# Kernel tuning notes

Measured on AMD Instinct MI355X. Metric: run time of the kernel, lower is better.

The kernel has to match this reference:

```python
import jax, jax.numpy as jnp
import numpy as np
from jax import lax

G = 16          # deform_groups
K = 9           # 3x3 kernel points
MAX_RES = 10.0  # max_residue_magnitude
PAD = 1         # stride=1, padding=1, dilation=1


def _leaky(x):
    return jnp.where(x >= 0, x, 0.1 * x)


def _conv3x3(x, w, b):
    y = lax.conv_general_dilated(x, w, (1, 1), ((PAD, PAD), (PAD, PAD)),
                                 dimension_numbers=('NCHW', 'OIHW', 'NCHW'))
    return y + b[None, :, None, None]


def _deform_conv2d(x, offset, mask, weight, bias):
    # x: [B,Cin,H,W]; offset: [B,2*G*K,H,W]; mask: [B,G*K,H,W]
    B, Cin, H, W = x.shape
    cpg = Cin // G
    Cout = weight.shape[0]
    # torchvision layout: [B, G, K, 2(y,x), H, W]
    off = offset.reshape(B, G, K, 2, H, W)
    ky = (jnp.arange(K) // 3 - PAD).astype(x.dtype).reshape(1, 1, K, 1, 1)
    kx = (jnp.arange(K) % 3 - PAD).astype(x.dtype).reshape(1, 1, K, 1, 1)
    py = jnp.arange(H, dtype=x.dtype).reshape(1, 1, 1, H, 1) + ky + off[:, :, :, 0]  # [B,G,K,H,W]
    px = jnp.arange(W, dtype=x.dtype).reshape(1, 1, 1, 1, W) + kx + off[:, :, :, 1]
    y0f = jnp.floor(py)
    x0f = jnp.floor(px)
    wy = py - y0f
    wx = px - x0f
    y0 = y0f.astype(jnp.int32)
    x0 = x0f.astype(jnp.int32)

    xf = x.reshape(B, G, cpg, H * W)
    # gather per (batch, group): xg [cpg, H*W], idx [K,H,W] -> [cpg,K,H,W]
    gather_fn = jax.vmap(jax.vmap(lambda xg, idx: jnp.take(xg, idx, axis=1)))

    def corner(yi, xi):
        valid = (yi >= 0) & (yi < H) & (xi >= 0) & (xi < W)   # zero padding outside
        idx = jnp.clip(yi, 0, H - 1) * W + jnp.clip(xi, 0, W - 1)
        v = gather_fn(xf, idx)                                # [B,G,cpg,K,H,W]
        return v * valid[:, :, None].astype(x.dtype)

    val = (corner(y0, x0) * ((1 - wy) * (1 - wx))[:, :, None]
           + corner(y0, x0 + 1) * ((1 - wy) * wx)[:, :, None]
           + corner(y0 + 1, x0) * (wy * (1 - wx))[:, :, None]
           + corner(y0 + 1, x0 + 1) * (wy * wx)[:, :, None])
    val = val * mask.reshape(B, G, 1, K, H, W)                # modulation
    wr = weight.reshape(Cout, G, cpg, K)
    return jnp.einsum('ogck,bgckhw->bohw', wr, val) + bias[None, :, None, None]


def _forward(x, extra_feat, flow_1, flow_2, w1, b1, w2, b2, w3, b3, w4, b4, dcn_w, dcn_b):
    ef = jnp.concatenate([extra_feat, flow_1, flow_2], axis=1)
    h = _leaky(_conv3x3(ef, w1, b1))
    h = _leaky(_conv3x3(h, w2, b2))
    h = _leaky(_conv3x3(h, w3, b3))
    out = _conv3x3(h, w4, b4)                 # [B, 27*G, H, W]
    o1, o2, m = jnp.split(out, 3, axis=1)
    offset = MAX_RES * jnp.tanh(jnp.concatenate([o1, o2], axis=1))
    off1, off2 = jnp.split(offset, 2, axis=1)
    rep = off1.shape[1] // 2
    off1 = off1 + jnp.tile(flow_1[:, ::-1], (1, rep, 1, 1))   # flip(1): (x,y)->(y,x)
    off2 = off2 + jnp.tile(flow_2[:, ::-1], (1, rep, 1, 1))
    offset = jnp.concatenate([off1, off2], axis=1)
    mask = jax.nn.sigmoid(m)
    return _deform_conv2d(x, offset, mask, dcn_w, dcn_b)


def setup_inputs() -> dict:
    key = jax.random.key(0)
    ks = jax.random.split(key, 10)
    B, H, W = 2, 128, 128
    Cin, Cout = 128, 64
    n = lambda k, s, sc=1.0: jax.random.normal(k, s, dtype=jnp.float32) * sc
    return {
        'x': n(ks[0], (B, Cin, H, W)),
        'extra_feat': n(ks[1], (B, 3 * Cout, H, W)),
        'flow_1': n(ks[2], (B, 2, H, W)),
        'flow_2': n(ks[3], (B, 2, H, W)),
        'w1': n(ks[4], (Cout, 3 * Cout + 4, 3, 3), 0.02), 'b1': jnp.zeros((Cout,), jnp.float32),
        'w2': n(ks[5], (Cout, Cout, 3, 3), 0.05), 'b2': jnp.zeros((Cout,), jnp.float32),
        'w3': n(ks[6], (Cout, Cout, 3, 3), 0.05), 'b3': jnp.zeros((Cout,), jnp.float32),
        'w4': n(ks[7], (27 * G, Cout, 3, 3), 0.01), 'b4': jnp.zeros((27 * G,), jnp.float32),
        'dcn_w': n(ks[8], (Cout, Cin, 3, 3), 0.05), 'dcn_b': jnp.zeros((Cout,), jnp.float32),
    }


def reference(x, extra_feat, flow_1, flow_2, w1, b1, w2, b2, w3, b3, w4, b4, dcn_w, dcn_b):
    return _forward(x, extra_feat, flow_1, flow_2, w1, b1, w2, b2, w3, b3, w4, b4, dcn_w, dcn_b)
```

## Files before the change

### kernel.cpp

```cpp
#include <hip/hip_runtime.h>
#include <math.h>

namespace {
constexpr int H = 128, W = 128, NB = 2;
constexpr int HW = H * W;
constexpr int WP = 130, HP = 130, HWP = WP * HP;
constexpr int NTHR = 256;
constexpr int DG = 16, CPG = 8, DCN_CIN = 128, DCN_COUT = 64;

constexpr size_t OFF_HA  = 0;
constexpr size_t OFF_HB  = 2163200;
constexpr size_t OFF_PIN = 4326400;
constexpr size_t OFF_O4  = 4194304;
constexpr size_t OFF_XT  = 0;
}

__global__ __launch_bounds__(NTHR) void prep_k(
    const float* __restrict__ ef, const float* __restrict__ f1,
    const float* __restrict__ f2,
    float* __restrict__ pin, float* __restrict__ hA, float* __restrict__ hB)
{
  constexpr int PACK_N  = NB * 196 * HW;
  constexpr int BORD_CH = NB * (196 + 64 + 64);
  constexpr int BORD_N  = BORD_CH * 516;
  const int total = PACK_N + BORD_N;
  for (int gid = blockIdx.x * NTHR + threadIdx.x; gid < total;
       gid += gridDim.x * NTHR) {
    if (gid < PACK_N) {
      const int b = gid / (196 * HW);
      const int r = gid - b * 196 * HW;
      const int c = r / HW;
      const int p = r - c * HW;
      const int y = p / W, x = p - y * W;
      float v;
      if (c < 192)      v = ef[(b * 192 + c) * HW + p];
      else if (c < 194) v = f1[(b * 2 + (c - 192)) * HW + p];
      else              v = f2[(b * 2 + (c - 194)) * HW + p];
      pin[(size_t)(b * 196 + c) * HWP + (y + 1) * WP + (x + 1)] = v;
    } else {
      const int k  = gid - PACK_N;
      const int ch = k / 516;
      const int e  = k - ch * 516;
      float* base;
      if (ch < NB * 196)            base = pin + (size_t)ch * HWP;
      else if (ch < NB * 196 + NB * 64) base = hA + (size_t)(ch - NB * 196) * HWP;
      else                          base = hB + (size_t)(ch - NB * 196 - NB * 64) * HWP;
      int off;
      if (e < 260) { const int rr = (e < 130) ? 0 : (HP - 1); off = rr * WP + (e % 130); }
      else { const int e2 = e - 260; const int y = 1 + (e2 & 127); off = y * WP + ((e2 < 128) ? 0 : (WP - 1)); }
      base[off] = 0.f;
    }
  }
}

template<int CIN, int COUT, int CC, int EPI>
__global__ __launch_bounds__(NTHR) void conv3x3_k(
    const float* __restrict__ in,
    const float* __restrict__ wt,
    const float* __restrict__ bias,
    const float* __restrict__ fl1, const float* __restrict__ fl2,
    float* __restrict__ out)
{
  constexpr int NST = 2;
  constexpr int HHW = 34, HN = HHW * HHW;
  constexpr int IN_E = NST * HN;
  constexpr int J_IN = (IN_E + NTHR - 1) / NTHR;
  constexpr int WT_E = CC * NST * 9;
  constexpr int J_WT = (WT_E + NTHR - 1) / NTHR;
  constexpr int R = CIN / NST;

  __shared__ float s_in[2][NST * HN];
  __shared__ float s_wt[2][CC * NST * 12];

  const int t    = threadIdx.x;
  const int tile = blockIdx.x;
  const int tx0  = (tile & 3) * 32, ty0 = (tile >> 2) * 32;
  const int oc0  = blockIdx.y * CC;
  const int b    = blockIdx.z;
  const int px0  = (t & 15) * 2;
  const int py0  = (t >> 4) * 2;

  const float* inB = in + (size_t)b * CIN * HWP;

  int iadr[J_IN]; bool ivl[J_IN];
  #pragma unroll
  for (int j = 0; j < J_IN; ++j) {
    const int idx = j * NTHR + t;
    ivl[j] = idx < IN_E;
    const int ii = idx / HN, rem = idx - ii * HN;
    const int hy = rem / HHW, hx = rem - hy * HHW;
    iadr[j] = ivl[j] ? (ii * HWP + (ty0 + hy) * WP + (tx0 + hx)) : 0;
  }
  int wadr[J_WT], wl[J_WT]; bool wvl[J_WT];
  #pragma unroll
  for (int j = 0; j < J_WT; ++j) {
    const int idx = j * NTHR + t;
    wvl[j] = idx < WT_E;
    const int o = idx / (NST * 9), r2 = idx - o * (NST * 9), ii = r2 / 9, k = r2 - ii * 9;
    wadr[j] = wvl[j] ? (((oc0 + o) * CIN + ii) * 9 + k) : 0;
    wl[j]   = wvl[j] ? ((o * NST + ii) * 12 + k) : 0;
  }

  float rin[J_IN], rwt[J_WT], acc[CC][4];
  #pragma unroll
  for (int o = 0; o < CC; ++o)
    #pragma unroll
    for (int p = 0; p < 4; ++p) acc[o][p] = 0.f;

  #pragma unroll
  for (int j = 0; j < J_IN; ++j) if (ivl[j]) rin[j] = inB[iadr[j]];
  #pragma unroll
  for (int j = 0; j < J_WT; ++j) if (wvl[j]) rwt[j] = wt[wadr[j]];

  for (int r = 0; r < R; ++r) {
    float* si = s_in[r & 1];
    float* sw = s_wt[r & 1];
    #pragma unroll
    for (int j = 0; j < J_IN; ++j) if (ivl[j]) si[j * NTHR + t] = rin[j];
    #pragma unroll
    for (int j = 0; j < J_WT; ++j) if (wvl[j]) sw[wl[j]] = rwt[j];
    __syncthreads();
    if (r + 1 < R) {
      const float* ip = inB + (size_t)(r + 1) * NST * HWP;
      const float* wp = wt + (size_t)(r + 1) * NST * 9;
      #pragma unroll
      for (int j = 0; j < J_IN; ++j) if (ivl[j]) rin[j] = ip[iadr[j]];
      #pragma unroll
      for (int j = 0; j < J_WT; ++j) if (wvl[j]) rwt[j] = wp[wadr[j]];
    }
    #pragma unroll
    for (int i = 0; i < NST; ++i) {
      float va[16];
      #pragma unroll
      for (int dy = 0; dy < 4; ++dy)
        #pragma unroll
        for (int dx = 0; dx < 4; ++dx)
          va[dy * 4 + dx] = si[i * HN + (py0 + dy) * HHW + (px0 + dx)];
      #pragma unroll
      for (int o = 0; o < CC; ++o) {
        const float* wr = &sw[(o * NST + i) * 12];
        float w[9];
        #pragma unroll
        for (int k = 0; k < 9; ++k) w[k] = wr[k];
        #pragma unroll
        for (int py = 0; py < 2; ++py)
          #pragma unroll
          for (int px = 0; px < 2; ++px) {
            float a = acc[o][py * 2 + px];
            #pragma unroll
            for (int ky = 0; ky < 3; ++ky)
              #pragma unroll
              for (int kx = 0; kx < 3; ++kx)
                a = fmaf(va[(py + ky) * 4 + (px + kx)], w[ky * 3 + kx], a);
            acc[o][py * 2 + px] = a;
          }
      }
    }
  }

  if (EPI == 2) {
    float flo[2][2][2][2];
    #pragma unroll
    for (int py = 0; py < 2; ++py)
      #pragma unroll
      for (int px = 0; px < 2; ++px) {
        const int pix = (ty0 + py0 + py) * W + (tx0 + px0 + px);
        flo[0][0][py][px] = fl1[(b * 2 + 1) * HW + pix];
        flo[0][1][py][px] = fl1[(b * 2 + 0) * HW + pix];
        flo[1][0][py][px] = fl2[(b * 2 + 1) * HW + pix];
        flo[1][1][py][px] = fl2[(b * 2 + 0) * HW + pix];
      }
    #pragma unroll
    for (int o = 0; o < CC; ++o) {
      const int oc = oc0 + o;
      const float bz = bias[oc];
      const int yx = oc & 1;
      const int sel = ((oc >> 1) / 9 >= 8) ? 1 : 0;
      #pragma unroll
      for (int py = 0; py < 2; ++py)
        #pragma unroll
        for (int px = 0; px < 2; ++px) {
          float rr = acc[o][py * 2 + px] + bz;
          if (oc < 288) rr = 10.f * tanhf(rr) + flo[sel][yx][py][px];
          else          rr = 1.f / (1.f + expf(-rr));
          const int pix = (ty0 + py0 + py) * W + (tx0 + px0 + px);
          out[((size_t)b * COUT + oc) * HW + pix] = rr;
        }
    }
  } else {
    #pragma unroll
    for (int o = 0; o < CC; ++o) {
      const int oc = oc0 + o;
      const float bz = bias[oc];
      #pragma unroll
      for (int py = 0; py < 2; ++py)
        #pragma unroll
        for (int px = 0; px < 2; ++px) {
          float rr = acc[o][py * 2 + px] + bz;
          rr = (rr >= 0.f) ? rr : 0.1f * rr;
          const int y = ty0 + py0 + py, x = tx0 + px0 + px;
          out[((size_t)b * COUT + oc) * HWP + (y + 1) * WP + (x + 1)] = rr;
        }
    }
  }
}

__global__ __launch_bounds__(NTHR) void xpose_k(
    const float* __restrict__ x, const float* __restrict__ db,
    float* __restrict__ xt, float* __restrict__ out)
{
  constexpr int XT_N  = NB * DG * HW;
  constexpr int OUT_N = NB * DCN_COUT * HW;
  const int total = XT_N + OUT_N;
  for (int gid = blockIdx.x * NTHR + threadIdx.x; gid < total;
       gid += gridDim.x * NTHR) {
    if (gid < XT_N) {
      const int b = gid / (DG * HW);
      const int r = gid - b * DG * HW;
      const int g = r / HW;
      const int p = r - g * HW;
      float4 v0, v1;
      const float* xs = x + ((size_t)(b * DCN_CIN) + g * CPG) * HW + p;
      v0.x = xs[0 * HW]; v0.y = xs[1 * HW]; v0.z = xs[2 * HW]; v0.w = xs[3 * HW];
      v1.x = xs[4 * HW]; v1.y = xs[5 * HW]; v1.z = xs[6 * HW]; v1.w = xs[7 * HW];
      float4* xd = (float4*)(xt + ((size_t)gid) * CPG);
      xd[0] = v0; xd[1] = v1;
    } else {
      const int k  = gid - XT_N;
      const int oc = (k / HW) & (DCN_COUT - 1);
      out[k] = db[oc];
    }
  }
}

template<int GPB>
__global__ __launch_bounds__(NTHR, 4) void deform_k(
    const float* __restrict__ xt,
    const float* __restrict__ o4,
    const float* __restrict__ dw,
    float* __restrict__ out)
{
  const int t    = threadIdx.x;
  const int tile = blockIdx.x;
  const int gc   = blockIdx.y;
  const int b    = blockIdx.z;
  const int lx   = t & 15, ly = t >> 4;
  const int hx   = (tile & 7) * 16 + lx;
  const int hy   = (tile >> 3) * 16 + ly;
  const int pix  = hy * W + hx;

  const float* ob = o4 + (size_t)(b * 432) * HW + pix;

  float acc[DCN_COUT];
  #pragma unroll
  for (int o = 0; o < DCN_COUT; ++o) acc[o] = 0.f;

  #pragma unroll 1
  for (int gi = 0; gi < GPB; ++gi) {
    const int g = gc * GPB + gi;
    const float* xg = xt + ((size_t)(b * DG + g)) * HW * CPG;

    #pragma unroll 1
    for (int k = 0; k < 9; ++k) {
      const int cb = g * 9 + k;
      const float oy = ob[(2 * cb + 0) * HW];
      const float ox = ob[(2 * cb + 1) * HW];
      const float mk = ob[(288 + cb) * HW];
      const float py  = (float)(hy + k / 3 - 1) + oy;
      const float pxx = (float)(hx + k % 3 - 1) + ox;
      const float y0f = floorf(py), x0f = floorf(pxx);
      const float wy = py - y0f, wx = pxx - x0f;
      const int y0 = (int)y0f, x0 = (int)x0f;
      const bool vy0 = (y0 >= 0) && (y0 < H);
      const bool vy1 = (y0 + 1 >= 0) && (y0 + 1 < H);
      const bool vx0 = (x0 >= 0) && (x0 < W);
      const bool vx1 = (x0 + 1 >= 0) && (x0 + 1 < W);
      const int cy0 = min(max(y0, 0), H - 1);
      const int cy1 = min(max(y0 + 1, 0), H - 1);
      const int cx0 = min(max(x0, 0), W - 1);
      const int cx1 = min(max(x0 + 1, 0), W - 1);
      const float w00 = (vy0 && vx0) ? (1.f - wy) * (1.f - wx) * mk : 0.f;
      const float w01 = (vy0 && vx1) ? (1.f - wy) * wx * mk : 0.f;
      const float w10 = (vy1 && vx0) ? wy * (1.f - wx) * mk : 0.f;
      const float w11 = (vy1 && vx1) ? wy * wx * mk : 0.f;

      const float4* p00 = (const float4*)(xg + (size_t)(cy0 * W + cx0) * CPG);
      const float4* p01 = (const float4*)(xg + (size_t)(cy0 * W + cx1) * CPG);
      const float4* p10 = (const float4*)(xg + (size_t)(cy1 * W + cx0) * CPG);
      const float4* p11 = (const float4*)(xg + (size_t)(cy1 * W + cx1) * CPG);
      const float4 a0 = p00[0], a1 = p00[1];
      const float4 b0 = p01[0], b1 = p01[1];
      const float4 c0 = p10[0], c1 = p10[1];
      const float4 d0 = p11[0], d1 = p11[1];

      float val[CPG];
      val[0] = fmaf(w00, a0.x, fmaf(w01, b0.x, fmaf(w10, c0.x, w11 * d0.x)));
      val[1] = fmaf(w00, a0.y, fmaf(w01, b0.y, fmaf(w10, c0.y, w11 * d0.y)));
      val[2] = fmaf(w00, a0.z, fmaf(w01, b0.z, fmaf(w10, c0.z, w11 * d0.z)));
      val[3] = fmaf(w00, a0.w, fmaf(w01, b0.w, fmaf(w10, c0.w, w11 * d0.w)));
      val[4] = fmaf(w00, a1.x, fmaf(w01, b1.x, fmaf(w10, c1.x, w11 * d1.x)));
      val[5] = fmaf(w00, a1.y, fmaf(w01, b1.y, fmaf(w10, c1.y, w11 * d1.y)));
      val[6] = fmaf(w00, a1.z, fmaf(w01, b1.z, fmaf(w10, c1.z, w11 * d1.z)));
      val[7] = fmaf(w00, a1.w, fmaf(w01, b1.w, fmaf(w10, c1.w, w11 * d1.w)));

      #pragma unroll
      for (int c = 0; c < CPG; ++c) {
        const float* wp = dw + (size_t)((g * CPG + c) * 9 + k);
        #pragma unroll
        for (int o = 0; o < DCN_COUT; ++o)
          acc[o] = fmaf(val[c], wp[(size_t)o * (DCN_CIN * 9)], acc[o]);
      }
    }
  }

  float* ot = out + (size_t)(b * DCN_COUT) * HW + pix;
  #pragma unroll
  for (int o = 0; o < DCN_COUT; ++o)
    atomicAdd(ot + (size_t)o * HW, acc[o]);
}

extern "C" void kernel_launch(void* const* d_in, const int* in_sizes, int n_in,
                              void* d_out, int out_size, void* d_ws, size_t ws_size,
                              hipStream_t stream) {
  const float* x     = (const float*)d_in[0];
  const float* ef    = (const float*)d_in[1];
  const float* fl1   = (const float*)d_in[2];
  const float* fl2   = (const float*)d_in[3];
  const float* w1    = (const float*)d_in[4];
  const float* b1    = (const float*)d_in[5];
  const float* w2    = (const float*)d_in[6];
  const float* b2    = (const float*)d_in[7];
  const float* w3    = (const float*)d_in[8];
  const float* b3    = (const float*)d_in[9];
  const float* w4    = (const float*)d_in[10];
  const float* b4    = (const float*)d_in[11];
  const float* dcn_w = (const float*)d_in[12];
  const float* dcn_b = (const float*)d_in[13];

  float* ws  = (float*)d_ws;
  float* hA  = ws + OFF_HA;
  float* hB  = ws + OFF_HB;
  float* pin = ws + OFF_PIN;
  float* o4  = ws + OFF_O4;
  float* xt  = ws + OFF_XT;

  const dim3 blk(NTHR);
  prep_k<<<2048, blk, 0, stream>>>(ef, fl1, fl2, pin, hA, hB);
  conv3x3_k<196, 64, 4, 1><<<dim3(16, 16, NB), blk, 0, stream>>>(
      pin, w1, b1, nullptr, nullptr, hA);
  conv3x3_k<64, 64, 4, 1><<<dim3(16, 16, NB), blk, 0, stream>>>(
      hA, w2, b2, nullptr, nullptr, hB);
  conv3x3_k<64, 64, 4, 1><<<dim3(16, 16, NB), blk, 0, stream>>>(
      hB, w3, b3, nullptr, nullptr, hA);
  conv3x3_k<64, 432, 16, 2><<<dim3(16, 27, NB), blk, 0, stream>>>(
      hA, w4, b4, fl1, fl2, o4);
  xpose_k<<<2048, blk, 0, stream>>>(x, dcn_b, xt, (float*)d_out);
  deform_k<2><<<dim3(64, 8, NB), blk, 0, stream>>>(xt, o4, dcn_w,
                                                   (float*)d_out);
}
```

Measured before the change: 873.2 us.

## Restructure deformable conv with shared-memory sampled values and per-wave output channels

Rewrites the deformable conv so each 512-thread block covers an 8x8 pixel tile across all groups. Waves cooperatively bilinear-sample one kernel point each into double-buffered shared memory, then each wave accumulates 8 output channels from the shared samples. This removes the atomicAdd reduction and the separate bias-initialisation pass, and cuts the per-thread accumulator count. In exchange it adds block-wide barriers per group and an uneven split in which wave 0 samples an extra kernel point.

```diff
diff --git a/kernel.cpp b/kernel.cpp
--- a/kernel.cpp
+++ b/kernel.cpp
@@ -206,117 +206,143 @@
 }
 
 __global__ __launch_bounds__(NTHR) void xpose_k(
-    const float* __restrict__ x, const float* __restrict__ db,
-    float* __restrict__ xt, float* __restrict__ out)
+    const float* __restrict__ x, float* __restrict__ xt)
 {
-  constexpr int XT_N  = NB * DG * HW;
-  constexpr int OUT_N = NB * DCN_COUT * HW;
-  const int total = XT_N + OUT_N;
-  for (int gid = blockIdx.x * NTHR + threadIdx.x; gid < total;
+  constexpr int XT_N = NB * DG * HW;
+  for (int gid = blockIdx.x * NTHR + threadIdx.x; gid < XT_N;
        gid += gridDim.x * NTHR) {
-    if (gid < XT_N) {
-      const int b = gid / (DG * HW);
-      const int r = gid - b * DG * HW;
-      const int g = r / HW;
-      const int p = r - g * HW;
-      float4 v0, v1;
-      const float* xs = x + ((size_t)(b * DCN_CIN) + g * CPG) * HW + p;
-      v0.x = xs[0 * HW]; v0.y = xs[1 * HW]; v0.z = xs[2 * HW]; v0.w = xs[3 * HW];
-      v1.x = xs[4 * HW]; v1.y = xs[5 * HW]; v1.z = xs[6 * HW]; v1.w = xs[7 * HW];
-      float4* xd = (float4*)(xt + ((size_t)gid) * CPG);
-      xd[0] = v0; xd[1] = v1;
-    } else {
-      const int k  = gid - XT_N;
-      const int oc = (k / HW) & (DCN_COUT - 1);
-      out[k] = db[oc];
-    }
-  }
-}
-
-template<int GPB>
-__global__ __launch_bounds__(NTHR, 4) void deform_k(
+    const int b = gid / (DG * HW);
+    const int r = gid - b * DG * HW;
+    const int g = r / HW;
+    const int p = r - g * HW;
+    float4 v0, v1;
+    const float* xs = x + ((size_t)(b * DCN_CIN) + g * CPG) * HW + p;
+    v0.x = xs[0 * HW]; v0.y = xs[1 * HW]; v0.z = xs[2 * HW]; v0.w = xs[3 * HW];
+    v1.x = xs[4 * HW]; v1.y = xs[5 * HW]; v1.z = xs[6 * HW]; v1.w = xs[7 * HW];
+    float4* xd = (float4*)(xt + ((size_t)gid) * CPG);
+    xd[0] = v0; xd[1] = v1;
+  }
+}
+
+__global__ __launch_bounds__(512, 4) void deform_k(
     const float* __restrict__ xt,
     const float* __restrict__ o4,
     const float* __restrict__ dw,
+    const float* __restrict__ db,
     float* __restrict__ out)
 {
+  constexpr int PXT = 64, VSTR = 76;
+  __shared__ float s_val[2][PXT * VSTR];
+
   const int t    = threadIdx.x;
   const int tile = blockIdx.x;
-  const int gc   = blockIdx.y;
-  const int b    = blockIdx.z;
-  const int lx   = t & 15, ly = t >> 4;
-  const int hx   = (tile & 7) * 16 + lx;
-  const int hy   = (tile >> 3) * 16 + ly;
-  const int pix  = hy * W + hx;
-
-  const float* ob = o4 + (size_t)(b * 432) * HW + pix;
-
-  float acc[DCN_COUT];
-  #pragma unroll
-  for (int o = 0; o < DCN_COUT; ++o) acc[o] = 0.f;
-
-  #pragma unroll 1
-  for (int gi = 0; gi < GPB; ++gi) {
-    const int g = gc * GPB + gi;
-    const float* xg = xt + ((size_t)(b * DG + g)) * HW * CPG;
-
-    #pragma unroll 1
-    for (int k = 0; k < 9; ++k) {
-      const int cb = g * 9 + k;
-      const float oy = ob[(2 * cb + 0) * HW];
-      const float ox = ob[(2 * cb + 1) * HW];
-      const float mk = ob[(288 + cb) * HW];
-      const float py  = (float)(hy + k / 3 - 1) + oy;
-      const float pxx = (float)(hx + k % 3 - 1) + ox;
-      const float y0f = floorf(py), x0f = floorf(pxx);
-      const float wy = py - y0f, wx = pxx - x0f;
-      const int y0 = (int)y0f, x0 = (int)x0f;
-      const bool vy0 = (y0 >= 0) && (y0 < H);
-      const bool vy1 = (y0 + 1 >= 0) && (y0 + 1 < H);
-      const bool vx0 = (x0 >= 0) && (x0 < W);
-      const bool vx1 = (x0 + 1 >= 0) && (x0 + 1 < W);
-      const int cy0 = min(max(y0, 0), H - 1);
-      const int cy1 = min(max(y0 + 1, 0), H - 1);
-      const int cx0 = min(max(x0, 0), W - 1);
-      const int cx1 = min(max(x0 + 1, 0), W - 1);
-      const float w00 = (vy0 && vx0) ? (1.f - wy) * (1.f - wx) * mk : 0.f;
-      const float w01 = (vy0 && vx1) ? (1.f - wy) * wx * mk : 0.f;
-      const float w10 = (vy1 && vx0) ? wy * (1.f - wx) * mk : 0.f;
-      const float w11 = (vy1 && vx1) ? wy * wx * mk : 0.f;
-
-      const float4* p00 = (const float4*)(xg + (size_t)(cy0 * W + cx0) * CPG);
-      const float4* p01 = (const float4*)(xg + (size_t)(cy0 * W + cx1) * CPG);
-      const float4* p10 = (const float4*)(xg + (size_t)(cy1 * W + cx0) * CPG);
-      const float4* p11 = (const float4*)(xg + (size_t)(cy1 * W + cx1) * CPG);
-      const float4 a0 = p00[0], a1 = p00[1];
-      const float4 b0 = p01[0], b1 = p01[1];
-      const float4 c0 = p10[0], c1 = p10[1];
-      const float4 d0 = p11[0], d1 = p11[1];
-
-      float val[CPG];
-      val[0] = fmaf(w00, a0.x, fmaf(w01, b0.x, fmaf(w10, c0.x, w11 * d0.x)));
-      val[1] = fmaf(w00, a0.y, fmaf(w01, b0.y, fmaf(w10, c0.y, w11 * d0.y)));
-      val[2] = fmaf(w00, a0.z, fmaf(w01, b0.z, fmaf(w10, c0.z, w11 * d0.z)));
-      val[3] = fmaf(w00, a0.w, fmaf(w01, b0.w, fmaf(w10, c0.w, w11 * d0.w)));
-      val[4] = fmaf(w00, a1.x, fmaf(w01, b1.x, fmaf(w10, c1.x, w11 * d1.x)));
-      val[5] = fmaf(w00, a1.y, fmaf(w01, b1.y, fmaf(w10, c1.y, w11 * d1.y)));
-      val[6] = fmaf(w00, a1.z, fmaf(w01, b1.z, fmaf(w10, c1.z, w11 * d1.z)));
-      val[7] = fmaf(w00, a1.w, fmaf(w01, b1.w, fmaf(w10, c1.w, w11 * d1.w)));
-
-      #pragma unroll
-      for (int c = 0; c < CPG; ++c) {
-        const float* wp = dw + (size_t)((g * CPG + c) * 9 + k);
-        #pragma unroll
-        for (int o = 0; o < DCN_COUT; ++o)
-          acc[o] = fmaf(val[c], wp[(size_t)o * (DCN_CIN * 9)], acc[o]);
+  const int b    = blockIdx.y;
+  const int tx0  = (tile & 15) * 8, ty0 = (tile >> 4) * 8;
+  const int lane = t & 63;
+  const int wv   = t >> 6;
+  const int sx   = tx0 + (lane & 7), sy = ty0 + (lane >> 3);
+  const int spix = sy * W + sx;
+
+  const float* o4b = o4 + (size_t)b * 432 * HW + spix;
+  const float* xtb = xt + (size_t)b * DG * HW * CPG;
+
+  float acc[8];
+  #pragma unroll
+  for (int o = 0; o < 8; ++o) acc[o] = 0.f;
+
+  auto sample = [&](int g, int k, int buf) {
+    const int cb = g * 9 + k;
+    const float oy = o4b[(2 * cb + 0) * HW];
+    const float ox = o4b[(2 * cb + 1) * HW];
+    const float mk = o4b[(288 + cb) * HW];
+    const float py  = (float)(sy + k / 3 - 1) + oy;
+    const float pxx = (float)(sx + k % 3 - 1) + ox;
+    const float y0f = floorf(py), x0f = floorf(pxx);
+    const float wy = py - y0f, wx = pxx - x0f;
+    const int y0 = (int)y0f, x0 = (int)x0f;
+    const bool vy0 = (y0 >= 0) && (y0 < H);
+    const bool vy1 = (y0 + 1 >= 0) && (y0 + 1 < H);
+    const bool vx0 = (x0 >= 0) && (x0 < W);
+    const bool vx1 = (x0 + 1 >= 0) && (x0 + 1 < W);
+    const int cy0 = min(max(y0, 0), H - 1);
+    const int cy1 = min(max(y0 + 1, 0), H - 1);
+    const int cx0 = min(max(x0, 0), W - 1);
+    const int cx1 = min(max(x0 + 1, 0), W - 1);
+    const float w00 = (vy0 && vx0) ? (1.f - wy) * (1.f - wx) * mk : 0.f;
+    const float w01 = (vy0 && vx1) ? (1.f - wy) * wx * mk : 0.f;
+    const float w10 = (vy1 && vx0) ? wy * (1.f - wx) * mk : 0.f;
+    const float w11 = (vy1 && vx1) ? wy * wx * mk : 0.f;
+
+    const float* xg = xtb + (size_t)g * HW * CPG;
+    const float4* p00 = (const float4*)(xg + (size_t)(cy0 * W + cx0) * CPG);
+    const float4* p01 = (const float4*)(xg + (size_t)(cy0 * W + cx1) * CPG);
+    const float4* p10 = (const float4*)(xg + (size_t)(cy1 * W + cx0) * CPG);
+    const float4* p11 = (const float4*)(xg + (size_t)(cy1 * W + cx1) * CPG);
+    const float4 a0 = p00[0], a1 = p00[1];
+    const float4 b0 = p01[0], b1 = p01[1];
+    const float4 c0 = p10[0], c1 = p10[1];
+    const float4 d0 = p11[0], d1 = p11[1];
+
+    float4 r0, r1;
+    r0.x = fmaf(w00, a0.x, fmaf(w01, b0.x, fmaf(w10, c0.x, w11 * d0.x)));
+    r0.y = fmaf(w00, a0.y, fmaf(w01, b0.y, fmaf(w10, c0.y, w11 * d0.y)));
+    r0.z = fmaf(w00, a0.z, fmaf(w01, b0.z, fmaf(w10, c0.z, w11 * d0.z)));
+    r0.w = fmaf(w00, a0.w, fmaf(w01, b0.w, fmaf(w10, c0.w, w11 * d0.w)));
+    r1.x = fmaf(w00, a1.x, fmaf(w01, b1.x, fmaf(w10, c1.x, w11 * d1.x)));
+    r1.y = fmaf(w00, a1.y, fmaf(w01, b1.y, fmaf(w10, c1.y, w11 * d1.y)));
+    r1.z = fmaf(w00, a1.z, fmaf(w01, b1.z, fmaf(w10, c1.z, w11 * d1.z)));
+    r1.w = fmaf(w00, a1.w, fmaf(w10 * 0.f + w01, b1.w, fmaf(w10, c1.w, w11 * d1.w)));
+    r1.w = fmaf(w00, a1.w, fmaf(w01, b1.w, fmaf(w10, c1.w, w11 * d1.w)));
+
+    float4* dst = (float4*)&s_val[buf][(lane) * VSTR + k * 8];
+    dst[0] = r0; dst[1] = r1;
+  };
+
+  auto sample_group = [&](int g, int buf) {
+    sample(g, wv, buf);
+    sample(g, wv + 0 == wv ? wv : wv, buf);
+  };
+
+  {
+    sample(0, wv, 0);
+    if (wv == 0) sample(0, 8, 0);
+  }
+  __syncthreads();
+
+  for (int g = 0; g < DG; ++g) {
+    const int buf = g & 1;
+    if (g + 1 < DG) {
+      sample(g + 1, wv, buf ^ 1);
+      if (wv == 0) sample(g + 1, 8, buf ^ 1);
+    }
+    float vv[72];
+    {
+      const float4* vp = (const float4*)&s_val[buf][lane * VSTR];
+      #pragma unroll
+      for (int j = 0; j < 18; ++j) {
+        const float4 v4 = vp[j];
+        vv[j * 4 + 0] = v4.x; vv[j * 4 + 1] = v4.y;
+        vv[j * 4 + 2] = v4.z; vv[j * 4 + 3] = v4.w;
       }
     }
-  }
-
-  float* ot = out + (size_t)(b * DCN_COUT) * HW + pix;
-  #pragma unroll
-  for (int o = 0; o < DCN_COUT; ++o)
-    atomicAdd(ot + (size_t)o * HW, acc[o]);
+    #pragma unroll
+    for (int o = 0; o < 8; ++o) {
+      const float* wb = dw + ((size_t)(wv * 8 + o) * DCN_CIN + g * CPG) * 9;
+      float a = acc[o];
+      #pragma unroll
+      for (int c = 0; c < CPG; ++c)
+        #pragma unroll
+        for (int k = 0; k < 9; ++k)
+          a = fmaf(vv[k * 8 + c], wb[c * 9 + k], a);
+      acc[o] = a;
+    }
+    __syncthreads();
+  }
+
+  float* ob2 = out + ((size_t)b * DCN_COUT + wv * 8) * HW + spix;
+  #pragma unroll
+  for (int o = 0; o < 8; ++o)
+    ob2[(size_t)o * HW] = acc[o] + db[wv * 8 + o];
 }
 
 extern "C" void kernel_launch(void* const* d_in, const int* in_sizes, int n_in,
@@ -354,7 +380,7 @@
       hB, w3, b3, nullptr, nullptr, hA);
   conv3x3_k<64, 432, 16, 2><<<dim3(16, 27, NB), blk, 0, stream>>>(
       hA, w4, b4, fl1, fl2, o4);
-  xpose_k<<<2048, blk, 0, stream>>>(x, dcn_b, xt, (float*)d_out);
-  deform_k<2><<<dim3(64, 8, NB), blk, 0, stream>>>(xt, o4, dcn_w,
-                                                   (float*)d_out);
-}
+  xpose_k<<<1024, blk, 0, stream>>>(x, xt);
+  deform_k<<<dim3(256, NB), dim3(512), 0, stream>>>(xt, o4, dcn_w, dcn_b,
+                                                    (float*)d_out);
+}
```

Measured after the change: 889.4 us. No clear change (+1.9%).
